# Kernel optimization log

Hardware: AMD Instinct MI355X
Metric: run time of the kernel (lower is better)

The kernel has to match this reference:

```python
import jax, jax.numpy as jnp
from jax import lax
import numpy as np

DIM = 256


def setup_inputs() -> dict:
    key = jax.random.key(0)
    ks = jax.random.split(key, 7)
    B, C, H, W = 16, DIM, 64, 64
    s = 0.02
    return {
        "x": jax.random.normal(ks[0], (B, C, H, W), dtype=jnp.float32),
        "qkv_w": jax.random.normal(ks[1], (3 * C, C), dtype=jnp.float32) * s,
        "qkv_b": jnp.zeros((3 * C,), dtype=jnp.float32),
        "proj_w": jax.random.normal(ks[2], (C, C), dtype=jnp.float32) * s,
        "proj_b": jnp.zeros((C,), dtype=jnp.float32),
        "conv_w": jax.random.normal(ks[3], (C, C, 3, 3), dtype=jnp.float32) * s,
        "conv_b": jnp.zeros((C,), dtype=jnp.float32),
    }


def reference(x, qkv_w, qkv_b, proj_w, proj_b, conv_w, conv_b):
    B, C, H, W = x.shape
    N = H * W
    scale = C ** (-0.5)
    # qkv on channels-last tokens: [B,N,3C]
    xp = x.transpose(0, 2, 3, 1).reshape(B, N, C)
    qkv = xp @ qkv_w.T + qkv_b
    q, k, v = jnp.split(qkv, 3, axis=-1)  # each [B,N,C]
    q = q.transpose(0, 2, 1)  # [B,C,N]
    v = v.transpose(0, 2, 1)  # [B,C,N]
    # channel attention: [B,C,C]
    attn = jax.nn.softmax(jnp.einsum('bcn,bnd->bcd', q, k) * scale, axis=-1)
    out = jnp.einsum('bcd,bdn->bcn', attn, v).transpose(0, 2, 1)  # [B,N,C]
    out = out @ proj_w.T + proj_b  # [B,N,C]
    # faithful to original: direct reshape [B,N,C] -> [B,C,H,W]
    attn_out = out.reshape(B, C, H, W)
    conv_out = lax.conv_general_dilated(
        x, conv_w, window_strides=(1, 1), padding=[(1, 1), (1, 1)],
        dimension_numbers=('NCHW', 'OIHW', 'NCHW'))
    conv_out = conv_out + conv_b[None, :, None, None]
    return attn_out + conv_out
```

## Files before the change

### kernel.cpp

```cpp
#include <hip/hip_runtime.h>
#include <hip/hip_bf16.h>

typedef unsigned short u16;
typedef __bf16 bf16x8 __attribute__((ext_vector_type(8)));
typedef float f32x4 __attribute__((ext_vector_type(4)));

#define BATCH 16
#define C 256
#define NTOK 4096
#define CN 1048576

__device__ __forceinline__ u16 f2b(float f) {
  __hip_bfloat16 h = __float2bfloat16(f);
  return __builtin_bit_cast(u16, h);
}
__device__ __forceinline__ float b2f(u16 u) {
  unsigned int x = ((unsigned int)u) << 16;
  return __builtin_bit_cast(float, x);
}

__device__ __forceinline__ void glds16(const u16* g, u16* l) {
  __builtin_amdgcn_global_load_lds(
      (const __attribute__((address_space(1))) unsigned int*)(g),
      (__attribute__((address_space(3))) unsigned int*)(l), 16, 0, 0);
}

__global__ __launch_bounds__(256) void prep_x_kernel(
    const float* __restrict__ x, u16* __restrict__ xbf, u16* __restrict__ xT,
    float* __restrict__ rws) {
  __shared__ float t[32][33];
  int b = blockIdx.z;
  int c0 = blockIdx.y * 32, n0 = blockIdx.x * 32;
  int tid = threadIdx.x;
  int i = tid >> 3, j4 = (tid & 7) * 4;
  const float* xb = x + (long)b * CN;
  float4 v = *(const float4*)(xb + (long)(c0 + i) * NTOK + n0 + j4);
  ushort4 bv;
  bv.x = f2b(v.x); bv.y = f2b(v.y); bv.z = f2b(v.z); bv.w = f2b(v.w);
  *(ushort4*)(xbf + (long)b * CN + (long)(c0 + i) * NTOK + n0 + j4) = bv;
  t[i][j4 + 0] = v.x; t[i][j4 + 1] = v.y; t[i][j4 + 2] = v.z; t[i][j4 + 3] = v.w;
  __syncthreads();
  ushort4 o;
  o.x = f2b(t[j4 + 0][i]); o.y = f2b(t[j4 + 1][i]);
  o.z = f2b(t[j4 + 2][i]); o.w = f2b(t[j4 + 3][i]);
  *(ushort4*)(xT + (long)b * CN + (long)(n0 + i) * C + c0 + j4) = o;
  if (tid < 32) {
    float s = 0.f;
#pragma unroll
    for (int j = 0; j < 32; ++j) s += t[tid][j];
    atomicAdd(&rws[b * C + c0 + tid], s);
  }
}

__global__ __launch_bounds__(256) void prep_w_kernel(
    const float* __restrict__ qkv_w, const float* __restrict__ proj_w,
    const float* __restrict__ conv_w, u16* __restrict__ Wq, u16* __restrict__ Wk,
    u16* __restrict__ WvT, u16* __restrict__ Pw, u16* __restrict__ cw,
    float* __restrict__ rws, u16* __restrict__ zbuf) {
  int idx = blockIdx.x * 256 + threadIdx.x;
  if (idx < 4096) rws[idx] = 0.f;
  if (idx < 256) zbuf[idx] = 0;
  if (idx < 65536) {
    Wq[idx] = f2b(qkv_w[idx]);
  } else if (idx < 131072) {
    int e = idx - 65536;
    Wk[e] = f2b(qkv_w[65536 + e]);
  } else if (idx < 196608) {
    int e = idx - 131072;
    int i = e >> 8, d = e & 255;
    WvT[e] = f2b(qkv_w[131072 + d * 256 + i]);
  } else if (idx < 262144) {
    int e = idx - 196608;
    Pw[e] = f2b(proj_w[e]);
  } else if (idx < 851968) {
    int e = idx - 262144;
    int o = e / 2304;
    int rem = e - o * 2304;
    int tap = rem >> 8, i = rem & 255;
    cw[e] = f2b(conv_w[o * 2304 + i * 9 + tap]);
  }
}

__global__ __launch_bounds__(512) void bias_uw_kernel(
    const float* __restrict__ qkv_w, const float* __restrict__ r,
    float* __restrict__ u, float* __restrict__ w) {
  int b = blockIdx.x, t = threadIdx.x;
  const float* rb = r + b * C;
  if (t < 256) {
    float s = 0.f;
    for (int i = 0; i < C; ++i) s += qkv_w[(256 + t) * 256 + i] * rb[i];
    u[b * C + t] = s;
  } else {
    int c = t - 256;
    float s = 0.f;
    for (int i = 0; i < C; ++i) s += qkv_w[c * 256 + i] * rb[i];
    w[b * C + c] = s;
  }
}

template <int EPI>
__global__ __launch_bounds__(256, 2) void gemm_glds_kernel(
    const u16* __restrict__ A, const u16* __restrict__ B, void* __restrict__ Cv,
    int K, int lda, int ldb, int ldc, int tilesN, long sA, long sB, long sC,
    float scale, const float* __restrict__ e1, const float* __restrict__ e2,
    const float* __restrict__ e3, const float* __restrict__ e4, int e34stride) {
  int b = blockIdx.z, ks = blockIdx.y;
  A += (long)b * sA + (long)ks * K;
  B += (long)b * sB + (long)ks * K;
  int ty = blockIdx.x / tilesN, tx = blockIdx.x % tilesN;
  int row0 = ty * 128, col0 = tx * 128;

  __shared__ u16 lA[2][4096];
  __shared__ u16 lB[2][4096];

  int tid = threadIdx.x;
  int lane = tid & 63, wv = tid >> 6;
  int wm = wv >> 1, wn = wv & 1;
  int fr = lane & 15, kq = lane >> 4;
  int kqs = kq ^ ((fr >> 1) & 3);

  int c0 = wv * 128 + lane, c1 = c0 + 64;
  int r0s = c0 >> 2, r1s = c1 >> 2;
  int ls0 = (c0 & 3) ^ ((r0s >> 1) & 3);
  int ls1 = (c1 & 3) ^ ((r1s >> 1) & 3);
  const u16* pA0 = A + (long)(row0 + r0s) * lda + ls0 * 8;
  const u16* pA1 = A + (long)(row0 + r1s) * lda + ls1 * 8;
  const u16* pB0 = B + (long)(col0 + r0s) * ldb + ls0 * 8;
  const u16* pB1 = B + (long)(col0 + r1s) * ldb + ls1 * 8;
  int dst0 = wv * 1024, dst1 = wv * 1024 + 512;

  f32x4 acc[4][4] = {};

  auto STAGE = [&](int buf, int t) {
    int k0 = t << 5;
    glds16(pA0 + k0, &lA[buf][dst0]);
    glds16(pA1 + k0, &lA[buf][dst1]);
    glds16(pB0 + k0, &lB[buf][dst0]);
    glds16(pB1 + k0, &lB[buf][dst1]);
  };
  auto COMPUTE = [&](int buf) {
    bf16x8 af[4], bfr[4];
#pragma unroll
    for (int m = 0; m < 4; ++m)
      af[m] = *(const bf16x8*)&lA[buf][(wm * 64 + m * 16 + fr) * 32 + kqs * 8];
#pragma unroll
    for (int n = 0; n < 4; ++n)
      bfr[n] = *(const bf16x8*)&lB[buf][(wn * 64 + n * 16 + fr) * 32 + kqs * 8];
#pragma unroll
    for (int m = 0; m < 4; ++m)
#pragma unroll
      for (int n = 0; n < 4; ++n)
        acc[m][n] = __builtin_amdgcn_mfma_f32_16x16x32_bf16(af[m], bfr[n], acc[m][n], 0, 0, 0);
  };

  int nk = K >> 5, cur = 0;
  STAGE(0, 0);
  __syncthreads();
  for (int t = 0; t < nk; ++t) {
    if (t + 1 < nk) STAGE(cur ^ 1, t + 1);
    COMPUTE(cur);
    __syncthreads();
    cur ^= 1;
  }

  if (EPI == 0) {
    float* Cb = (float*)Cv + ((long)b * gridDim.y + ks) * sC;
#pragma unroll
    for (int m = 0; m < 4; ++m)
#pragma unroll
      for (int n = 0; n < 4; ++n)
#pragma unroll
        for (int r = 0; r < 4; ++r) {
          int gr = row0 + wm * 64 + m * 16 + kq * 4 + r;
          int gc = col0 + wn * 64 + n * 16 + fr;
          Cb[(long)gr * ldc + gc] = acc[m][n][r];
        }
  } else if (EPI == 1) {
    __hip_bfloat16* Cb = (__hip_bfloat16*)Cv + (long)b * sC;
#pragma unroll
    for (int m = 0; m < 4; ++m)
#pragma unroll
      for (int n = 0; n < 4; ++n)
#pragma unroll
        for (int r = 0; r < 4; ++r) {
          int gr = row0 + wm * 64 + m * 16 + kq * 4 + r;
          int gc = col0 + wn * 64 + n * 16 + fr;
          Cb[(long)gr * ldc + gc] = __float2bfloat16(acc[m][n][r]);
        }
  } else if (EPI == 2) {
    float* Cb = (float*)Cv + (long)b * sC;
    const float* ub = e3 + (long)b * e34stride;
    const float* wb = e4 + (long)b * e34stride;
#pragma unroll
    for (int m = 0; m < 4; ++m)
#pragma unroll
      for (int n = 0; n < 4; ++n)
#pragma unroll
        for (int r = 0; r < 4; ++r) {
          int gr = row0 + wm * 64 + m * 16 + kq * 4 + r;
          int gc = col0 + wn * 64 + n * 16 + fr;
          float v = acc[m][n][r] + e1[gr] * ub[gc] + e2[gc] * wb[gr] +
                    4096.0f * e1[gr] * e2[gc];
          Cb[(long)gr * ldc + gc] = v * scale;
        }
  }
}

__global__ __launch_bounds__(256) void reduceG_kernel(
    const float* __restrict__ Gp, u16* __restrict__ G) {
  int b = blockIdx.y;
  int e = blockIdx.x * 1024 + threadIdx.x * 4;
  const float* base = Gp + (long)b * 262144;
  float4 s = *(const float4*)(base + e);
#pragma unroll
  for (int sl = 1; sl < 4; ++sl) {
    float4 v = *(const float4*)(base + sl * 65536 + e);
    s.x += v.x; s.y += v.y; s.z += v.z; s.w += v.w;
  }
  ushort4 o;
  o.x = f2b(s.x); o.y = f2b(s.y); o.z = f2b(s.z); o.w = f2b(s.w);
  *(ushort4*)(G + (long)b * 65536 + e) = o;
}

__global__ __launch_bounds__(256) void softmax_kernel(const float* __restrict__ S,
                                                      u16* __restrict__ attnT) {
  int row = blockIdx.x;
  int t = threadIdx.x;
  float v = S[(long)row * C + t];
  __shared__ float red[256];
  red[t] = v; __syncthreads();
  for (int st = 128; st > 0; st >>= 1) {
    if (t < st) red[t] = fmaxf(red[t], red[t + st]);
    __syncthreads();
  }
  float mx = red[0];
  __syncthreads();
  float e = __expf(v - mx);
  red[t] = e; __syncthreads();
  for (int st = 128; st > 0; st >>= 1) {
    if (t < st) red[t] += red[t + st];
    __syncthreads();
  }
  float inv = 1.0f / red[0];
  int b = row >> 8, c = row & 255;
  attnT[(long)b * 65536 + t * 256 + c] = f2b(e * inv);
}

__global__ __launch_bounds__(256) void cbias_kernel(const u16* __restrict__ M,
                                                    const float* __restrict__ qkv_b,
                                                    const float* __restrict__ proj_b,
                                                    float* __restrict__ cb) {
  int b = blockIdx.x, j = threadIdx.x;
  const u16* m = M + (long)b * 65536 + (long)j * 256;
  float s = 0.f;
  for (int d = 0; d < C; ++d) s += b2f(m[d]) * qkv_b[512 + d];
  cb[b * C + j] = proj_b[j] + s;
}

__global__ __launch_bounds__(256, 2) void convattn_kernel(
    const u16* __restrict__ xT, const u16* __restrict__ cw,
    const u16* __restrict__ W2, const u16* __restrict__ zbuf,
    const float* __restrict__ conv_b, const float* __restrict__ cb,
    float* __restrict__ out) {
  int b = blockIdx.y;
  int to = blockIdx.x >> 5, tn = blockIdx.x & 31;
  int row0 = to * 128, col0 = tn * 128;
  const u16* xTb = xT + (long)b * CN;
  const u16* W2b = W2 + (long)b * 65536;

  __shared__ u16 lA[2][4096];
  __shared__ u16 lB[2][4096];

  int tid = threadIdx.x;
  int lane = tid & 63, wv = tid >> 6;
  int wm = wv >> 1, wn = wv & 1;
  int fr = lane & 15, kq = lane >> 4;
  int kqs = kq ^ ((fr >> 1) & 3);

  int c0 = wv * 128 + lane, c1 = c0 + 64;
  int r0s = c0 >> 2, r1s = c1 >> 2;
  int ls0 = (c0 & 3) ^ ((r0s >> 1) & 3);
  int ls1 = (c1 & 3) ^ ((r1s >> 1) & 3);
  int dst0 = wv * 1024, dst1 = wv * 1024 + 512;

  const u16* pA0 = cw + (long)(row0 + r0s) * 2304 + ls0 * 8;
  const u16* pA1 = cw + (long)(row0 + r1s) * 2304 + ls1 * 8;
  int t0 = col0 + r0s, t1 = col0 + r1s;
  int h0 = t0 >> 6, w0 = t0 & 63, h1 = t1 >> 6, w1 = t1 & 63;
  const u16* pB0 = xTb + (long)t0 * 256 + ls0 * 8;
  const u16* pB1 = xTb + (long)t1 * 256 + ls1 * 8;
  int nb = col0 >> 8, jb = col0 & 255;
  const u16* qA0 = xTb + (long)((row0 + r0s) * 16 + nb) * 256 + ls0 * 8;
  const u16* qA1 = xTb + (long)((row0 + r1s) * 16 + nb) * 256 + ls1 * 8;
  const u16* qB0 = W2b + (long)(jb + r0s) * 256 + ls0 * 8;
  const u16* qB1 = W2b + (long)(jb + r1s) * 256 + ls1 * 8;

  f32x4 accC[4][4] = {};
  f32x4 accY[4][4] = {};

  auto STAGE_CONV = [&](int buf, int t) {
    int tap = t >> 3, i0 = (t & 7) << 5;
    int dh = tap / 3 - 1, dw = tap % 3 - 1;
    long dt = (long)(dh * 64 + dw) * 256 + i0;
    glds16(pA0 + tap * 256 + i0, &lA[buf][dst0]);
    glds16(pA1 + tap * 256 + i0, &lA[buf][dst1]);
    bool v0 = ((unsigned)(h0 + dh) < 64u) && ((unsigned)(w0 + dw) < 64u);
    bool v1 = ((unsigned)(h1 + dh) < 64u) && ((unsigned)(w1 + dw) < 64u);
    const u16* s0 = v0 ? pB0 + dt : zbuf + ls0 * 8;
    const u16* s1 = v1 ? pB1 + dt : zbuf + ls1 * 8;
    glds16(s0, &lB[buf][dst0]);
    glds16(s1, &lB[buf][dst1]);
  };
  auto STAGE_ATTN = [&](int buf, int t) {
    int k0 = t << 5;
    glds16(qA0 + k0, &lA[buf][dst0]);
    glds16(qA1 + k0, &lA[buf][dst1]);
    glds16(qB0 + k0, &lB[buf][dst0]);
    glds16(qB1 + k0, &lB[buf][dst1]);
  };
  auto COMPUTE = [&](int buf, f32x4 (&acc)[4][4]) {
    bf16x8 af[4], bfr[4];
#pragma unroll
    for (int m = 0; m < 4; ++m)
      af[m] = *(const bf16x8*)&lA[buf][(wm * 64 + m * 16 + fr) * 32 + kqs * 8];
#pragma unroll
    for (int n = 0; n < 4; ++n)
      bfr[n] = *(const bf16x8*)&lB[buf][(wn * 64 + n * 16 + fr) * 32 + kqs * 8];
#pragma unroll
    for (int m = 0; m < 4; ++m)
#pragma unroll
      for (int n = 0; n < 4; ++n)
        acc[m][n] = __builtin_amdgcn_mfma_f32_16x16x32_bf16(af[m], bfr[n], acc[m][n], 0, 0, 0);
  };

  int cur = 0;
  STAGE_CONV(0, 0);
  __syncthreads();
  for (int t = 0; t < 72; ++t) {
    if (t < 71) STAGE_CONV(cur ^ 1, t + 1);
    else STAGE_ATTN(cur ^ 1, 0);
    COMPUTE(cur, accC);
    __syncthreads();
    cur ^= 1;
  }
  for (int t = 0; t < 8; ++t) {
    if (t < 7) STAGE_ATTN(cur ^ 1, t + 1);
    COMPUTE(cur, accY);
    __syncthreads();
    cur ^= 1;
  }

  float* ob = out + (long)b * CN;
  const float* cbb = cb + b * C;
#pragma unroll
  for (int m = 0; m < 4; ++m)
#pragma unroll
    for (int nn = 0; nn < 4; ++nn)
#pragma unroll
      for (int r = 0; r < 4; ++r) {
        int go = row0 + wm * 64 + m * 16 + kq * 4 + r;
        int cc = wn * 64 + nn * 16 + fr;
        int gn = col0 + cc;
        ob[(long)go * NTOK + gn] =
            accC[m][nn][r] + accY[m][nn][r] + conv_b[go] + cbb[jb + cc];
      }
}

extern "C" void kernel_launch(void* const* d_in, const int* in_sizes, int n_in,
                              void* d_out, int out_size, void* d_ws, size_t ws_size,
                              hipStream_t stream) {
  const float* x = (const float*)d_in[0];
  const float* qkv_w = (const float*)d_in[1];
  const float* qkv_b = (const float*)d_in[2];
  const float* proj_w = (const float*)d_in[3];
  const float* proj_b = (const float*)d_in[4];
  const float* conv_w = (const float*)d_in[5];
  const float* conv_b = (const float*)d_in[6];
  float* out = (float*)d_out;
  char* ws = (char*)d_ws;

  u16* xbf = (u16*)(ws);
  u16* xT = (u16*)(ws + 33554432);
  u16* Gbf = (u16*)(ws + 67108864);
  float* Gpart = (float*)(ws + 69206016);
  u16* T1bf = (u16*)(ws + 69206016);
  float* Sf = (float*)(ws + 71303168);
  u16* attnT = (u16*)(ws + 75497472);
  u16* Mbf = (u16*)(ws + 77594624);
  u16* W2bf = (u16*)(ws + 79691776);
  u16* Wq = (u16*)(ws + 85983232);
  u16* Wk = (u16*)(ws + 86114304);
  u16* WvT = (u16*)(ws + 86245376);
  u16* Pw = (u16*)(ws + 86376448);
  u16* cw = (u16*)(ws + 86507520);
  float* rws = (float*)(ws + 87687168);
  float* uws = (float*)(ws + 87703552);
  float* wws = (float*)(ws + 87719936);
  float* cb = (float*)(ws + 87736320);
  u16* zbuf = (u16*)(ws + 87752704);

  prep_w_kernel<<<3328, 256, 0, stream>>>(qkv_w, proj_w, conv_w, Wq, Wk, WvT,
                                          Pw, cw, rws, zbuf);
  prep_x_kernel<<<dim3(128, 8, BATCH), 256, 0, stream>>>(x, xbf, xT, rws);
  bias_uw_kernel<<<BATCH, 512, 0, stream>>>(qkv_w, rws, uws, wws);

  gemm_glds_kernel<0><<<dim3(4, 4, BATCH), 256, 0, stream>>>(
      xbf, xbf, Gpart, 1024, 4096, 4096, 256, 2, CN, CN, 65536,
      0.f, nullptr, nullptr, nullptr, nullptr, 0);
  reduceG_kernel<<<dim3(64, BATCH), 256, 0, stream>>>(Gpart, Gbf);

  gemm_glds_kernel<1><<<dim3(4, 1, BATCH), 256, 0, stream>>>(
      Wq, Gbf, T1bf, 256, 256, 256, 256, 2, 0, 65536, 65536,
      0.f, nullptr, nullptr, nullptr, nullptr, 0);
  gemm_glds_kernel<2><<<dim3(4, 1, BATCH), 256, 0, stream>>>(
      T1bf, Wk, Sf, 256, 256, 256, 256, 2, 65536, 0, 65536,
      0.0625f, qkv_b, qkv_b + 256, uws, wws, 256);

  softmax_kernel<<<BATCH * C, 256, 0, stream>>>(Sf, attnT);

  gemm_glds_kernel<1><<<dim3(4, 1, BATCH), 256, 0, stream>>>(
      Pw, attnT, Mbf, 256, 256, 256, 256, 2, 0, 65536, 65536,
      0.f, nullptr, nullptr, nullptr, nullptr, 0);
  cbias_kernel<<<BATCH, 256, 0, stream>>>(Mbf, qkv_b, proj_b, cb);
  gemm_glds_kernel<1><<<dim3(4, 1, BATCH), 256, 0, stream>>>(
      Mbf, WvT, W2bf, 256, 256, 256, 256, 2, 65536, 0, 65536,
      0.f, nullptr, nullptr, nullptr, nullptr, 0);

  convattn_kernel<<<dim3(64, BATCH), 256, 0, stream>>>(xT, cw, W2bf, zbuf,
                                                       conv_b, cb, out);
}
```

Measured before the change: 250.0 us.

## Enlarge convattn tiles to 256x256 with 8 waves and triple-buffered LDS pipeline

The fused conv+attention GEMM kernel now has each 512-thread block compute all 256 output channels for 256 tokens, replacing 128x128 tiles. Conv and attention accumulators are merged into one. Loads use a three-stage LDS ring with explicit vmcnt waits and raw barriers, and MFMA sections get raised wave priority. The aim is more operand reuse per LDS load and less global traffic, plus overlap of loads with compute. In exchange the grid drops to 256 blocks, roughly one per CU, and register pressure rises with 32 accumulator tiles per wave.

```diff
diff --git a/kernel.cpp b/kernel.cpp
--- a/kernel.cpp
+++ b/kernel.cpp
@@ -257,113 +257,122 @@
   cb[b * C + j] = proj_b[j] + s;
 }
 
-__global__ __launch_bounds__(256, 2) void convattn_kernel(
+__global__ __launch_bounds__(512, 2) void convattn_kernel(
     const u16* __restrict__ xT, const u16* __restrict__ cw,
     const u16* __restrict__ W2, const u16* __restrict__ zbuf,
     const float* __restrict__ conv_b, const float* __restrict__ cb,
     float* __restrict__ out) {
   int b = blockIdx.y;
-  int to = blockIdx.x >> 5, tn = blockIdx.x & 31;
-  int row0 = to * 128, col0 = tn * 128;
+  int tn = blockIdx.x;
+  int col0 = tn * 256;
   const u16* xTb = xT + (long)b * CN;
   const u16* W2b = W2 + (long)b * 65536;
 
-  __shared__ u16 lA[2][4096];
-  __shared__ u16 lB[2][4096];
+  __shared__ u16 lA[3][8192];
+  __shared__ u16 lB[3][8192];
 
   int tid = threadIdx.x;
-  int lane = tid & 63, wv = tid >> 6;
-  int wm = wv >> 1, wn = wv & 1;
+  int lane = tid & 63, w = tid >> 6;
+  int wr = w >> 2, wc = w & 3;
   int fr = lane & 15, kq = lane >> 4;
   int kqs = kq ^ ((fr >> 1) & 3);
 
-  int c0 = wv * 128 + lane, c1 = c0 + 64;
-  int r0s = c0 >> 2, r1s = c1 >> 2;
-  int ls0 = (c0 & 3) ^ ((r0s >> 1) & 3);
-  int ls1 = (c1 & 3) ^ ((r1s >> 1) & 3);
-  int dst0 = wv * 1024, dst1 = wv * 1024 + 512;
-
-  const u16* pA0 = cw + (long)(row0 + r0s) * 2304 + ls0 * 8;
-  const u16* pA1 = cw + (long)(row0 + r1s) * 2304 + ls1 * 8;
-  int t0 = col0 + r0s, t1 = col0 + r1s;
-  int h0 = t0 >> 6, w0 = t0 & 63, h1 = t1 >> 6, w1 = t1 & 63;
-  const u16* pB0 = xTb + (long)t0 * 256 + ls0 * 8;
-  const u16* pB1 = xTb + (long)t1 * 256 + ls1 * 8;
-  int nb = col0 >> 8, jb = col0 & 255;
-  const u16* qA0 = xTb + (long)((row0 + r0s) * 16 + nb) * 256 + ls0 * 8;
-  const u16* qA1 = xTb + (long)((row0 + r1s) * 16 + nb) * 256 + ls1 * 8;
-  const u16* qB0 = W2b + (long)(jb + r0s) * 256 + ls0 * 8;
-  const u16* qB1 = W2b + (long)(jb + r1s) * 256 + ls1 * 8;
-
-  f32x4 accC[4][4] = {};
-  f32x4 accY[4][4] = {};
-
-  auto STAGE_CONV = [&](int buf, int t) {
-    int tap = t >> 3, i0 = (t & 7) << 5;
-    int dh = tap / 3 - 1, dw = tap % 3 - 1;
-    long dt = (long)(dh * 64 + dw) * 256 + i0;
-    glds16(pA0 + tap * 256 + i0, &lA[buf][dst0]);
-    glds16(pA1 + tap * 256 + i0, &lA[buf][dst1]);
-    bool v0 = ((unsigned)(h0 + dh) < 64u) && ((unsigned)(w0 + dw) < 64u);
-    bool v1 = ((unsigned)(h1 + dh) < 64u) && ((unsigned)(w1 + dw) < 64u);
-    const u16* s0 = v0 ? pB0 + dt : zbuf + ls0 * 8;
-    const u16* s1 = v1 ? pB1 + dt : zbuf + ls1 * 8;
-    glds16(s0, &lB[buf][dst0]);
-    glds16(s1, &lB[buf][dst1]);
+  int rA0 = w * 32 + (lane >> 2);
+  int rA1 = rA0 + 16;
+  int slot = (lane & 3) ^ ((lane >> 3) & 3);
+  int dA0 = w * 1024, dA1 = dA0 + 512;
+
+  const u16* awA0 = cw + (long)rA0 * 2304 + slot * 8;
+  const u16* awA1 = cw + (long)rA1 * 2304 + slot * 8;
+  int t0 = col0 + rA0, t1 = col0 + rA1;
+  int h0 = t0 >> 6, w0_ = t0 & 63, h1 = t1 >> 6, w1_ = t1 & 63;
+  const u16* pB0 = xTb + (long)t0 * 256 + slot * 8;
+  const u16* pB1 = xTb + (long)t1 * 256 + slot * 8;
+  const u16* zsrc = zbuf + slot * 8;
+  const u16* aq0 = xTb + (long)(rA0 * 16 + tn) * 256 + slot * 8;
+  const u16* aq1 = xTb + (long)(rA1 * 16 + tn) * 256 + slot * 8;
+  const u16* qb0 = W2b + (long)rA0 * 256 + slot * 8;
+  const u16* qb1 = W2b + (long)rA1 * 256 + slot * 8;
+
+  f32x4 acc[8][4] = {};
+
+  u16* A0 = lA[0]; u16* A1 = lA[1]; u16* A2 = lA[2];
+  u16* B0 = lB[0]; u16* B1 = lB[1]; u16* B2 = lB[2];
+
+  auto STAGE = [&](u16* bA, u16* bB, int t) {
+    if (t < 72) {
+      int tap = t >> 3, i0 = (t & 7) << 5;
+      int dh = tap / 3 - 1, dw = tap % 3 - 1;
+      glds16(awA0 + tap * 256 + i0, bA + dA0);
+      glds16(awA1 + tap * 256 + i0, bA + dA1);
+      long sh = (long)(dh * 64 + dw) * 256 + i0;
+      bool v0 = ((unsigned)(h0 + dh) < 64u) && ((unsigned)(w0_ + dw) < 64u);
+      bool v1 = ((unsigned)(h1 + dh) < 64u) && ((unsigned)(w1_ + dw) < 64u);
+      glds16(v0 ? pB0 + sh : zsrc, bB + dA0);
+      glds16(v1 ? pB1 + sh : zsrc, bB + dA1);
+    } else {
+      int c0k = (t - 72) << 5;
+      glds16(aq0 + c0k, bA + dA0);
+      glds16(aq1 + c0k, bA + dA1);
+      glds16(qb0 + c0k, bB + dA0);
+      glds16(qb1 + c0k, bB + dA1);
+    }
   };
-  auto STAGE_ATTN = [&](int buf, int t) {
-    int k0 = t << 5;
-    glds16(qA0 + k0, &lA[buf][dst0]);
-    glds16(qA1 + k0, &lA[buf][dst1]);
-    glds16(qB0 + k0, &lB[buf][dst0]);
-    glds16(qB1 + k0, &lB[buf][dst1]);
+  auto COMPUTE = [&](const u16* bA, const u16* bB) {
+    bf16x8 af[8], bv[4];
+#pragma unroll
+    for (int mf = 0; mf < 8; ++mf)
+      af[mf] = *(const bf16x8*)(bA + (wr * 128 + mf * 16 + fr) * 32 + kqs * 8);
+#pragma unroll
+    for (int nf = 0; nf < 4; ++nf)
+      bv[nf] = *(const bf16x8*)(bB + (wc * 64 + nf * 16 + fr) * 32 + kqs * 8);
+    __builtin_amdgcn_s_setprio(1);
+#pragma unroll
+    for (int mf = 0; mf < 8; ++mf)
+#pragma unroll
+      for (int nf = 0; nf < 4; ++nf)
+        acc[mf][nf] = __builtin_amdgcn_mfma_f32_16x16x32_bf16(af[mf], bv[nf], acc[mf][nf], 0, 0, 0);
+    __builtin_amdgcn_s_setprio(0);
   };
-  auto COMPUTE = [&](int buf, f32x4 (&acc)[4][4]) {
-    bf16x8 af[4], bfr[4];
-#pragma unroll
-    for (int m = 0; m < 4; ++m)
-      af[m] = *(const bf16x8*)&lA[buf][(wm * 64 + m * 16 + fr) * 32 + kqs * 8];
-#pragma unroll
-    for (int n = 0; n < 4; ++n)
-      bfr[n] = *(const bf16x8*)&lB[buf][(wn * 64 + n * 16 + fr) * 32 + kqs * 8];
-#pragma unroll
-    for (int m = 0; m < 4; ++m)
-#pragma unroll
-      for (int n = 0; n < 4; ++n)
-        acc[m][n] = __builtin_amdgcn_mfma_f32_16x16x32_bf16(af[m], bfr[n], acc[m][n], 0, 0, 0);
-  };
-
-  int cur = 0;
-  STAGE_CONV(0, 0);
-  __syncthreads();
-  for (int t = 0; t < 72; ++t) {
-    if (t < 71) STAGE_CONV(cur ^ 1, t + 1);
-    else STAGE_ATTN(cur ^ 1, 0);
-    COMPUTE(cur, accC);
-    __syncthreads();
-    cur ^= 1;
-  }
-  for (int t = 0; t < 8; ++t) {
-    if (t < 7) STAGE_ATTN(cur ^ 1, t + 1);
-    COMPUTE(cur, accY);
-    __syncthreads();
-    cur ^= 1;
+
+  STAGE(A0, B0, 0);
+  STAGE(A1, B1, 1);
+  asm volatile("s_waitcnt vmcnt(4)" ::: "memory");
+  __builtin_amdgcn_sched_barrier(0);
+  __builtin_amdgcn_s_barrier();
+  __builtin_amdgcn_sched_barrier(0);
+
+  for (int t = 0; t < 80; ++t) {
+    if (t + 2 < 80) {
+      STAGE(A2, B2, t + 2);
+      COMPUTE(A0, B0);
+      asm volatile("s_waitcnt vmcnt(4)" ::: "memory");
+    } else {
+      COMPUTE(A0, B0);
+      asm volatile("s_waitcnt vmcnt(0)" ::: "memory");
+    }
+    __builtin_amdgcn_sched_barrier(0);
+    __builtin_amdgcn_s_barrier();
+    __builtin_amdgcn_sched_barrier(0);
+    u16* tA = A0; A0 = A1; A1 = A2; A2 = tA;
+    u16* tB = B0; B0 = B1; B1 = B2; B2 = tB;
   }
 
   float* ob = out + (long)b * CN;
   const float* cbb = cb + b * C;
 #pragma unroll
-  for (int m = 0; m < 4; ++m)
-#pragma unroll
-    for (int nn = 0; nn < 4; ++nn)
-#pragma unroll
-      for (int r = 0; r < 4; ++r) {
-        int go = row0 + wm * 64 + m * 16 + kq * 4 + r;
-        int cc = wn * 64 + nn * 16 + fr;
-        int gn = col0 + cc;
-        ob[(long)go * NTOK + gn] =
-            accC[m][nn][r] + accY[m][nn][r] + conv_b[go] + cbb[jb + cc];
-      }
+  for (int mf = 0; mf < 8; ++mf) {
+    int go = wr * 128 + mf * 16 + kq * 4;
+#pragma unroll
+    for (int nf = 0; nf < 4; ++nf) {
+      int cc = wc * 64 + nf * 16 + fr;
+      float cbv = cbb[cc];
+#pragma unroll
+      for (int r = 0; r < 4; ++r)
+        ob[(long)(go + r) * NTOK + col0 + cc] =
+            acc[mf][nf][r] + conv_b[go + r] + cbv;
+    }
+  }
 }
 
 extern "C" void kernel_launch(void* const* d_in, const int* in_sizes, int n_in,
@@ -426,6 +435,6 @@
       Mbf, WvT, W2bf, 256, 256, 256, 256, 2, 65536, 0, 65536,
       0.f, nullptr, nullptr, nullptr, nullptr, 0);
 
-  convattn_kernel<<<dim3(64, BATCH), 256, 0, stream>>>(xT, cw, W2bf, zbuf,
+  convattn_kernel<<<dim3(16, BATCH), 512, 0, stream>>>(xT, cw, W2bf, zbuf,
                                                        conv_b, cb, out);
 }
```

Measured after the change: 582.0 us. 133% more time.

## Triple-buffer conv+attn GEMM loop with single accumulator and vmcnt-based barriers

Applied to the files above, without the earlier changes.

Replaces the double-buffered LDS pipeline with a three-stage ring, so loads are issued two iterations ahead and waited on with partial vmcnt instead of full __syncthreads. The conv and attention K-loops are merged into one 80-step loop that accumulates into a single register tile, which removes the second 64-float accumulator and lowers register pressure. MFMA sections are also wrapped in s_setprio. LDS use grows by half, which could limit occupancy at 2 blocks per SM. The vmcnt counts must stay exactly right for correctness.

```diff
diff --git a/kernel.cpp b/kernel.cpp
--- a/kernel.cpp
+++ b/kernel.cpp
@@ -263,13 +263,14 @@
     const float* __restrict__ conv_b, const float* __restrict__ cb,
     float* __restrict__ out) {
   int b = blockIdx.y;
-  int to = blockIdx.x >> 5, tn = blockIdx.x & 31;
+  int to = blockIdx.x >> 5;
+  int tn = blockIdx.x & 31;
   int row0 = to * 128, col0 = tn * 128;
   const u16* xTb = xT + (long)b * CN;
   const u16* W2b = W2 + (long)b * 65536;
 
-  __shared__ u16 lA[2][4096];
-  __shared__ u16 lB[2][4096];
+  __shared__ u16 lA[3][4096];
+  __shared__ u16 lB[3][4096];
 
   int tid = threadIdx.x;
   int lane = tid & 63, wv = tid >> 6;
@@ -286,39 +287,39 @@
   const u16* pA0 = cw + (long)(row0 + r0s) * 2304 + ls0 * 8;
   const u16* pA1 = cw + (long)(row0 + r1s) * 2304 + ls1 * 8;
   int t0 = col0 + r0s, t1 = col0 + r1s;
-  int h0 = t0 >> 6, w0 = t0 & 63, h1 = t1 >> 6, w1 = t1 & 63;
+  int h0 = t0 >> 6, w0_ = t0 & 63, h1 = t1 >> 6, w1_ = t1 & 63;
   const u16* pB0 = xTb + (long)t0 * 256 + ls0 * 8;
   const u16* pB1 = xTb + (long)t1 * 256 + ls1 * 8;
+  const u16* zs0 = zbuf + ls0 * 8;
+  const u16* zs1 = zbuf + ls1 * 8;
   int nb = col0 >> 8, jb = col0 & 255;
   const u16* qA0 = xTb + (long)((row0 + r0s) * 16 + nb) * 256 + ls0 * 8;
   const u16* qA1 = xTb + (long)((row0 + r1s) * 16 + nb) * 256 + ls1 * 8;
   const u16* qB0 = W2b + (long)(jb + r0s) * 256 + ls0 * 8;
   const u16* qB1 = W2b + (long)(jb + r1s) * 256 + ls1 * 8;
 
-  f32x4 accC[4][4] = {};
-  f32x4 accY[4][4] = {};
-
-  auto STAGE_CONV = [&](int buf, int t) {
-    int tap = t >> 3, i0 = (t & 7) << 5;
-    int dh = tap / 3 - 1, dw = tap % 3 - 1;
-    long dt = (long)(dh * 64 + dw) * 256 + i0;
-    glds16(pA0 + tap * 256 + i0, &lA[buf][dst0]);
-    glds16(pA1 + tap * 256 + i0, &lA[buf][dst1]);
-    bool v0 = ((unsigned)(h0 + dh) < 64u) && ((unsigned)(w0 + dw) < 64u);
-    bool v1 = ((unsigned)(h1 + dh) < 64u) && ((unsigned)(w1 + dw) < 64u);
-    const u16* s0 = v0 ? pB0 + dt : zbuf + ls0 * 8;
-    const u16* s1 = v1 ? pB1 + dt : zbuf + ls1 * 8;
-    glds16(s0, &lB[buf][dst0]);
-    glds16(s1, &lB[buf][dst1]);
+  f32x4 acc[4][4] = {};
+
+  auto STAGE = [&](int buf, int t) {
+    if (t < 72) {
+      int tap = t >> 3, i0 = (t & 7) << 5;
+      int dh = tap / 3 - 1, dw = tap % 3 - 1;
+      glds16(pA0 + tap * 256 + i0, &lA[buf][dst0]);
+      glds16(pA1 + tap * 256 + i0, &lA[buf][dst1]);
+      long sh = (long)(dh * 64 + dw) * 256 + i0;
+      bool v0 = ((unsigned)(h0 + dh) < 64u) && ((unsigned)(w0_ + dw) < 64u);
+      bool v1 = ((unsigned)(h1 + dh) < 64u) && ((unsigned)(w1_ + dw) < 64u);
+      glds16(v0 ? pB0 + sh : zs0, &lB[buf][dst0]);
+      glds16(v1 ? pB1 + sh : zs1, &lB[buf][dst1]);
+    } else {
+      int k0 = (t - 72) << 5;
+      glds16(qA0 + k0, &lA[buf][dst0]);
+      glds16(qA1 + k0, &lA[buf][dst1]);
+      glds16(qB0 + k0, &lB[buf][dst0]);
+      glds16(qB1 + k0, &lB[buf][dst1]);
+    }
   };
-  auto STAGE_ATTN = [&](int buf, int t) {
-    int k0 = t << 5;
-    glds16(qA0 + k0, &lA[buf][dst0]);
-    glds16(qA1 + k0, &lA[buf][dst1]);
-    glds16(qB0 + k0, &lB[buf][dst0]);
-    glds16(qB1 + k0, &lB[buf][dst1]);
-  };
-  auto COMPUTE = [&](int buf, f32x4 (&acc)[4][4]) {
+  auto COMPUTE = [&](int buf) {
     bf16x8 af[4], bfr[4];
 #pragma unroll
     for (int m = 0; m < 4; ++m)
@@ -326,44 +327,54 @@
 #pragma unroll
     for (int n = 0; n < 4; ++n)
       bfr[n] = *(const bf16x8*)&lB[buf][(wn * 64 + n * 16 + fr) * 32 + kqs * 8];
+    __builtin_amdgcn_s_setprio(1);
 #pragma unroll
     for (int m = 0; m < 4; ++m)
 #pragma unroll
       for (int n = 0; n < 4; ++n)
         acc[m][n] = __builtin_amdgcn_mfma_f32_16x16x32_bf16(af[m], bfr[n], acc[m][n], 0, 0, 0);
+    __builtin_amdgcn_s_setprio(0);
   };
 
+  STAGE(0, 0);
+  STAGE(1, 1);
+  asm volatile("s_waitcnt vmcnt(4)" ::: "memory");
+  __builtin_amdgcn_sched_barrier(0);
+  __builtin_amdgcn_s_barrier();
+  __builtin_amdgcn_sched_barrier(0);
+
   int cur = 0;
-  STAGE_CONV(0, 0);
-  __syncthreads();
-  for (int t = 0; t < 72; ++t) {
-    if (t < 71) STAGE_CONV(cur ^ 1, t + 1);
-    else STAGE_ATTN(cur ^ 1, 0);
-    COMPUTE(cur, accC);
-    __syncthreads();
-    cur ^= 1;
-  }
-  for (int t = 0; t < 8; ++t) {
-    if (t < 7) STAGE_ATTN(cur ^ 1, t + 1);
-    COMPUTE(cur, accY);
-    __syncthreads();
-    cur ^= 1;
+  for (int t = 0; t < 80; ++t) {
+    int nxt = cur + 2; if (nxt >= 3) nxt -= 3;
+    if (t + 2 < 80) {
+      STAGE(nxt, t + 2);
+      COMPUTE(cur);
+      asm volatile("s_waitcnt vmcnt(4)" ::: "memory");
+    } else {
+      COMPUTE(cur);
+      asm volatile("s_waitcnt vmcnt(0)" ::: "memory");
+    }
+    __builtin_amdgcn_sched_barrier(0);
+    __builtin_amdgcn_s_barrier();
+    __builtin_amdgcn_sched_barrier(0);
+    cur = (cur + 1 == 3) ? 0 : cur + 1;
   }
 
   float* ob = out + (long)b * CN;
   const float* cbb = cb + b * C;
 #pragma unroll
-  for (int m = 0; m < 4; ++m)
-#pragma unroll
-    for (int nn = 0; nn < 4; ++nn)
-#pragma unroll
-      for (int r = 0; r < 4; ++r) {
-        int go = row0 + wm * 64 + m * 16 + kq * 4 + r;
-        int cc = wn * 64 + nn * 16 + fr;
-        int gn = col0 + cc;
-        ob[(long)go * NTOK + gn] =
-            accC[m][nn][r] + accY[m][nn][r] + conv_b[go] + cbb[jb + cc];
-      }
+  for (int m = 0; m < 4; ++m) {
+    int go = row0 + wm * 64 + m * 16 + kq * 4;
+#pragma unroll
+    for (int nn = 0; nn < 4; ++nn) {
+      int cc = wn * 64 + nn * 16 + fr;
+      float cbv = cbb[jb + cc];
+#pragma unroll
+      for (int r = 0; r < 4; ++r)
+        ob[(long)(go + r) * NTOK + col0 + cc] =
+            acc[m][nn][r] + conv_b[go + r] + cbv;
+    }
+  }
 }
 
 extern "C" void kernel_launch(void* const* d_in, const int* in_sizes, int n_in,
```

Measured after the change: 260.5 us. 4.2% more time.
